# Kernel optimization log

Measured on AMD Instinct MI355X. Metric: run time of the kernel, lower is better.

The kernel has to match this reference:

```python
import jax, jax.numpy as jnp
import numpy as np

BATCH, TOK, DIM, OUT = 4, 2048, 4096, 4096
E, R, TOP_K = 8, 16, 2
SCALING = 16.0 / R  # lora_alpha / r


def setup_inputs() -> dict:
    key = jax.random.key(0)
    ks = jax.random.split(key, 6)
    return {
        "x": jax.random.normal(ks[0], (BATCH, TOK, DIM), dtype=jnp.float32),
        "W_base": jax.random.normal(ks[1], (OUT, DIM), dtype=jnp.float32) / np.sqrt(DIM),
        "b_base": jax.random.normal(ks[2], (OUT,), dtype=jnp.float32) * 0.01,
        "W_gate": jax.random.normal(ks[3], (E, DIM), dtype=jnp.float32) * 0.01,
        "A": jax.random.normal(ks[4], (E, R, DIM), dtype=jnp.float32) / np.sqrt(DIM),
        "B": jax.random.normal(ks[5], (OUT, OUT // OUT * R * 0 + R), dtype=jnp.float32)[None].repeat(E, 0) * 0.0 + jax.random.normal(ks[5], (E, OUT, R), dtype=jnp.float32) * 0.02,
    }


def reference(x, W_base, b_base, W_gate, A, B):
    # Base frozen linear: [B,N,D] @ [D,O] -> [B,N,O]
    result = jnp.einsum("bnd,od->bno", x, W_base) + b_base
    # Gating
    logits = jnp.einsum("bnd,ed->bne", x, W_gate)
    probs = jax.nn.softmax(logits.astype(jnp.float32), axis=-1)  # fp32 softmax
    top_p, top_i = jax.lax.top_k(probs, TOP_K)  # [B,N,K]
    top_p = top_p / jnp.sum(top_p, axis=-1, keepdims=True)  # top_k > 1 branch
    top_p = top_p.astype(x.dtype)
    # Scatter top-k probs back to dense [B,N,E] routing weights
    route_w = jnp.sum(jax.nn.one_hot(top_i, E, dtype=x.dtype) * top_p[..., None], axis=-2)
    # Per-expert LoRA: down-project all tokens for all experts (r is small),
    # weight by routing, then up-project and sum over experts.
    h = jnp.einsum("bnd,erd->bner", x, A)          # [B,N,E,r]
    hw = h * route_w[..., None]                      # mask/combine weighting
    delta = jnp.einsum("bner,eor->bno", hw, B)      # [B,N,O]
    return result + delta * SCALING
```

## Files before the change

kernel.cpp:

```cpp
#include <hip/hip_runtime.h>
#include <hip/hip_bf16.h>
#include <cstdint>

#define TOKENS 8192
#define DIM_   4096
#define OUTD   4096
#define NE     8
#define NR     16
#define LORA_COLS (NE*NR)
#define KCAT  (DIM_ + LORA_COLS)
#define NTILES (KCAT/64)
#define HSPLIT 8
#define HKC    (DIM_/HSPLIT)

typedef __attribute__((ext_vector_type(8))) short short8;
typedef __attribute__((ext_vector_type(4))) float f32x4;

__device__ __forceinline__ unsigned short f2bf(float f) {
  union { float f; unsigned u; } v; v.f = f;
  unsigned r = v.u + 0x7FFFu + ((v.u >> 16) & 1u);
  return (unsigned short)(r >> 16);
}
__device__ __forceinline__ float bf2f(unsigned short u) {
  union { unsigned u; float f; } v; v.u = ((unsigned)u) << 16; return v.f;
}

__device__ __forceinline__ void load_lds16(const void* g, void* l) {
  auto gp = reinterpret_cast<const __attribute__((address_space(1))) unsigned int*>(
      reinterpret_cast<uintptr_t>(g));
  auto lp = reinterpret_cast<__attribute__((address_space(3))) unsigned int*>(
      reinterpret_cast<uintptr_t>(l));
  __builtin_amdgcn_global_load_lds(gp, lp, 16, 0, 0);
}

#define BAR() asm volatile("s_barrier" ::: "memory")
#define LGKM(N) do { asm volatile("s_waitcnt lgkmcnt(" #N ")" ::: "memory"); \
                     __builtin_amdgcn_sched_barrier(0); } while (0)
#define VMW(N) asm volatile("s_waitcnt vmcnt(" #N ")" ::: "memory")
#define SB0() __builtin_amdgcn_sched_barrier(0)

__global__ __launch_bounds__(256) void fused_prep_kernel(
    const float* __restrict__ x, const float* __restrict__ Wg,
    const float* __restrict__ W, const float* __restrict__ Bm,
    const float* __restrict__ Am, unsigned short* __restrict__ Wcat,
    unsigned short* __restrict__ Acat, unsigned short* __restrict__ Xcat,
    int* __restrict__ ridx, float* __restrict__ rw, float scaling) {
  __shared__ float red[32 * 257];
  __shared__ float lg[32];
  int tid = threadIdx.x;
  int bb = blockIdx.x;
  if (bb < OUTD) {
    const float4* src = (const float4*)(W + (size_t)bb * DIM_);
    unsigned short* dst = Wcat + (size_t)bb * KCAT;
#pragma unroll
    for (int j = 0; j < DIM_ / 1024; ++j) {
      float4 v = src[j * 256 + tid];
      ushort4 o; o.x = f2bf(v.x); o.y = f2bf(v.y); o.z = f2bf(v.z); o.w = f2bf(v.w);
      *(ushort4*)(dst + (size_t)(j * 256 + tid) * 4) = o;
    }
    if (tid < LORA_COLS) {
      int e = tid >> 4, r = tid & 15;
      dst[DIM_ + tid] = f2bf(scaling * Bm[((size_t)e * OUTD + bb) * NR + r]);
    }
    return;
  }
  if (bb < OUTD + LORA_COLS) {
    int i = bb - OUTD;
    const float4* src = (const float4*)(Am + (size_t)i * DIM_);
    unsigned short* dst = Acat + (size_t)i * DIM_;
#pragma unroll
    for (int j = 0; j < DIM_ / 1024; ++j) {
      float4 v = src[j * 256 + tid];
      ushort4 o; o.x = f2bf(v.x); o.y = f2bf(v.y); o.z = f2bf(v.z); o.w = f2bf(v.w);
      *(ushort4*)(dst + (size_t)(j * 256 + tid) * 4) = o;
    }
    return;
  }
  int t0 = (bb - OUTD - LORA_COLS) * 4;
  float acc[4][8];
#pragma unroll
  for (int ti = 0; ti < 4; ++ti)
#pragma unroll
    for (int e = 0; e < 8; ++e) acc[ti][e] = 0.f;
  const float4* x4 = (const float4*)x;
  const float4* wg4 = (const float4*)Wg;
#pragma unroll
  for (int j = 0; j < 4; ++j) {
    int dpos = j * 256 + tid;
    float4 wg[8];
#pragma unroll
    for (int e = 0; e < 8; ++e) wg[e] = wg4[e * 1024 + dpos];
#pragma unroll
    for (int ti = 0; ti < 4; ++ti) {
      float4 v = x4[(size_t)(t0 + ti) * 1024 + dpos];
      ushort4 o; o.x = f2bf(v.x); o.y = f2bf(v.y); o.z = f2bf(v.z); o.w = f2bf(v.w);
      *(ushort4*)&Xcat[(size_t)(t0 + ti) * KCAT + (size_t)dpos * 4] = o;
#pragma unroll
      for (int e = 0; e < 8; ++e)
        acc[ti][e] += v.x * wg[e].x + v.y * wg[e].y + v.z * wg[e].z + v.w * wg[e].w;
    }
  }
#pragma unroll
  for (int p = 0; p < 32; ++p) red[p * 257 + tid] = acc[p >> 3][p & 7];
  __syncthreads();
  {
    int p = tid >> 3, part = tid & 7;
    float s = 0.f;
#pragma unroll
    for (int i = 0; i < 32; ++i) s += red[p * 257 + part * 32 + i];
    s += __shfl_xor(s, 1);
    s += __shfl_xor(s, 2);
    s += __shfl_xor(s, 4);
    if (part == 0) lg[p] = s;
  }
  __syncthreads();
  if (tid < 4) {
    float l[8];
#pragma unroll
    for (int e = 0; e < 8; ++e) l[e] = lg[tid * 8 + e];
    int i0 = 0; float m0 = l[0];
#pragma unroll
    for (int e = 1; e < 8; ++e) if (l[e] > m0) { m0 = l[e]; i0 = e; }
    int i1 = -1; float m1 = -3.4e38f;
#pragma unroll
    for (int e = 0; e < 8; ++e) if (e != i0 && l[e] > m1) { m1 = l[e]; i1 = e; }
    float w0 = 1.0f / (1.0f + expf(m1 - m0));
    int t = t0 + tid;
    ridx[t * 2] = i0; ridx[t * 2 + 1] = i1;
    rw[t * 2] = w0;  rw[t * 2 + 1] = 1.0f - w0;
  }
}

template <int MODE>
__global__ __launch_bounds__(256) void gemm_kernel(
    const unsigned short* __restrict__ Aop, const unsigned short* __restrict__ Bop,
    float* __restrict__ Cout, unsigned short* __restrict__ CoutBf,
    const float* __restrict__ bias, const int* __restrict__ ridx,
    const float* __restrict__ rw,
    int M, int N, int K, int lda, int ldb, int ldc) {
  __shared__ __align__(16) unsigned short lsA[128 * 32];
  __shared__ __align__(16) unsigned short lsB[128 * 32];
  int tid = threadIdx.x;
  int lane = tid & 63, wave = tid >> 6;
  int wm = wave >> 1, wn = wave & 1;
  int row0 = blockIdx.x * 128, col0 = blockIdx.y * 128;

  f32x4 acc[4][4];
#pragma unroll
  for (int a = 0; a < 4; ++a)
#pragma unroll
    for (int b = 0; b < 4; ++b) acc[a][b] = (f32x4){0.f, 0.f, 0.f, 0.f};

  int lrow = lane >> 2;
  int lcol = (lane & 3) << 3;
  int fr = lane & 15, fk = (lane >> 4) << 3;

  const unsigned short* gA0 = Aop + (size_t)(row0 + wave * 32 + lrow) * lda + lcol;
  const unsigned short* gA1 = Aop + (size_t)(row0 + wave * 32 + 16 + lrow) * lda + lcol;
  const unsigned short* gB0 = Bop + (size_t)(col0 + wave * 32 + lrow) * ldb + lcol;
  const unsigned short* gB1 = Bop + (size_t)(col0 + wave * 32 + 16 + lrow) * ldb + lcol;

  for (int k0 = 0; k0 < K; k0 += 32) {
    load_lds16(gA0 + k0, lsA + wave * 1024);
    load_lds16(gA1 + k0, lsA + wave * 1024 + 512);
    load_lds16(gB0 + k0, lsB + wave * 1024);
    load_lds16(gB1 + k0, lsB + wave * 1024 + 512);
    __syncthreads();
    short8 af[4], bfr[4];
#pragma unroll
    for (int mi = 0; mi < 4; ++mi)
      af[mi] = *(const short8*)&lsA[(wm * 64 + mi * 16 + fr) * 32 + fk];
#pragma unroll
    for (int ni = 0; ni < 4; ++ni)
      bfr[ni] = *(const short8*)&lsB[(wn * 64 + ni * 16 + fr) * 32 + fk];
#pragma unroll
    for (int mi = 0; mi < 4; ++mi)
#pragma unroll
      for (int ni = 0; ni < 4; ++ni)
        acc[mi][ni] = __builtin_amdgcn_mfma_f32_16x16x32_bf16(af[mi], bfr[ni], acc[mi][ni], 0, 0, 0);
    __syncthreads();
  }

  int fg = lane >> 4;
  if (MODE == 0) {
#pragma unroll
    for (int ni = 0; ni < 4; ++ni) {
      int col = col0 + wn * 64 + ni * 16 + fr;
      float bv = bias[col];
#pragma unroll
      for (int mi = 0; mi < 4; ++mi)
#pragma unroll
        for (int j = 0; j < 4; ++j) {
          int row = row0 + wm * 64 + mi * 16 + fg * 4 + j;
          Cout[(size_t)row * ldc + col] = acc[mi][ni][j] + bv;
        }
    }
  } else {
#pragma unroll
    for (int mi = 0; mi < 4; ++mi)
#pragma unroll
      for (int j = 0; j < 4; ++j) {
        int row = row0 + wm * 64 + mi * 16 + fg * 4 + j;
        int i0 = ridx[row * 2], i1 = ridx[row * 2 + 1];
        float w0 = rw[row * 2], w1 = rw[row * 2 + 1];
#pragma unroll
        for (int ni = 0; ni < 4; ++ni) {
          int col = wn * 64 + ni * 16 + fr;
          int e = col >> 4;
          float w = (e == i0) ? w0 : ((e == i1) ? w1 : 0.f);
          CoutBf[(size_t)row * ldc + col] = f2bf(w * acc[mi][ni][j]);
        }
      }
  }
}

__global__ __launch_bounds__(256) void gemm_h_sk_kernel(
    const unsigned short* __restrict__ Aop,
    const unsigned short* __restrict__ Bop,
    unsigned short* __restrict__ Hpart) {
  __shared__ __align__(16) unsigned short lsA[128 * 32];
  __shared__ __align__(16) unsigned short lsB[128 * 32];
  int tid = threadIdx.x;
  int lane = tid & 63, wave = tid >> 6;
  int wm = wave >> 1, wn = wave & 1;
  int row0 = blockIdx.x * 128;
  int s = blockIdx.y;
  int kbeg = s * HKC;

  f32x4 acc[4][4];
#pragma unroll
  for (int a = 0; a < 4; ++a)
#pragma unroll
    for (int b = 0; b < 4; ++b) acc[a][b] = (f32x4){0.f, 0.f, 0.f, 0.f};

  int lrow = lane >> 2;
  int lcol = (lane & 3) << 3;
  int fr = lane & 15, fk = (lane >> 4) << 3;

  const unsigned short* gA0 = Aop + (size_t)(row0 + wave * 32 + lrow) * KCAT + lcol;
  const unsigned short* gA1 = Aop + (size_t)(row0 + wave * 32 + 16 + lrow) * KCAT + lcol;
  const unsigned short* gB0 = Bop + (size_t)(wave * 32 + lrow) * DIM_ + lcol;
  const unsigned short* gB1 = Bop + (size_t)(wave * 32 + 16 + lrow) * DIM_ + lcol;

  for (int k0 = kbeg; k0 < kbeg + HKC; k0 += 32) {
    load_lds16(gA0 + k0, lsA + wave * 1024);
    load_lds16(gA1 + k0, lsA + wave * 1024 + 512);
    load_lds16(gB0 + k0, lsB + wave * 1024);
    load_lds16(gB1 + k0, lsB + wave * 1024 + 512);
    __syncthreads();
    short8 af[4], bfr[4];
#pragma unroll
    for (int mi = 0; mi < 4; ++mi)
      af[mi] = *(const short8*)&lsA[(wm * 64 + mi * 16 + fr) * 32 + fk];
#pragma unroll
    for (int ni = 0; ni < 4; ++ni)
      bfr[ni] = *(const short8*)&lsB[(wn * 64 + ni * 16 + fr) * 32 + fk];
#pragma unroll
    for (int mi = 0; mi < 4; ++mi)
#pragma unroll
      for (int ni = 0; ni < 4; ++ni)
        acc[mi][ni] = __builtin_amdgcn_mfma_f32_16x16x32_bf16(af[mi], bfr[ni], acc[mi][ni], 0, 0, 0);
    __syncthreads();
  }

  int fg = lane >> 4;
  unsigned short* outp = Hpart + (size_t)s * TOKENS * 128;
#pragma unroll
  for (int ni = 0; ni < 4; ++ni) {
    int col = wn * 64 + ni * 16 + fr;
#pragma unroll
    for (int mi = 0; mi < 4; ++mi)
#pragma unroll
      for (int j = 0; j < 4; ++j) {
        int row = row0 + wm * 64 + mi * 16 + fg * 4 + j;
        outp[(size_t)row * 128 + col] = f2bf(acc[mi][ni][j]);
      }
  }
}

__global__ __launch_bounds__(256) void h_combine_kernel(
    const unsigned short* __restrict__ Hpart, const int* __restrict__ ridx,
    const float* __restrict__ rw, unsigned short* __restrict__ Xcat) {
  int gid = blockIdx.x * 256 + threadIdx.x;
  int t = gid >> 7, c = gid & 127;
  float s = 0.f;
#pragma unroll
  for (int i = 0; i < HSPLIT; ++i) s += bf2f(Hpart[(size_t)i * TOKENS * 128 + gid]);
  int e = c >> 4;
  int i0 = ridx[t * 2], i1 = ridx[t * 2 + 1];
  float w = (e == i0) ? rw[t * 2] : ((e == i1) ? rw[t * 2 + 1] : 0.f);
  Xcat[(size_t)t * KCAT + DIM_ + c] = f2bf(w * s);
}

#define RD_A4(dst, base, ks, mi0) do { \
  dst[0] = *(const short8*)((base) + (((mi0)+0)*2+(ks))*1024); \
  dst[1] = *(const short8*)((base) + (((mi0)+1)*2+(ks))*1024); \
  dst[2] = *(const short8*)((base) + (((mi0)+2)*2+(ks))*1024); \
  dst[3] = *(const short8*)((base) + (((mi0)+3)*2+(ks))*1024); } while (0)
#define RD_B4(dst, base, ks) do { \
  dst[0] = *(const short8*)((base) + 0*2048 + (ks)*1024); \
  dst[1] = *(const short8*)((base) + 1*2048 + (ks)*1024); \
  dst[2] = *(const short8*)((base) + 2*2048 + (ks)*1024); \
  dst[3] = *(const short8*)((base) + 3*2048 + (ks)*1024); } while (0)
#define MFMA_H(a4, b4, m0, mo) do { \
  __builtin_amdgcn_s_setprio(1); \
  _Pragma("unroll") \
  for (int mi = 0; mi < 2; ++mi) { \
    _Pragma("unroll") \
    for (int ni = 0; ni < 4; ++ni) { \
      acc[(m0)+(mo)+mi][ni] = __builtin_amdgcn_mfma_f32_16x16x32_bf16( \
          b4[ni], a4[(mo)+mi], acc[(m0)+(mo)+mi][ni], 0, 0, 0); } } \
  __builtin_amdgcn_s_setprio(0); } while (0)
#define STAGE(srcp, kofs, dst) do { \
  load_lds16((srcp) + (kofs), (dst)); \
  load_lds16((srcp) + (kofs) + 32, (dst) + 1024); } while (0)

__global__ __launch_bounds__(512, 2) void gemm256_kernel(
    const unsigned short* __restrict__ Aop,
    const unsigned short* __restrict__ Bop,
    float* __restrict__ Cout, const float* __restrict__ bias) {
  extern __shared__ char lds[];
  const int tid = threadIdx.x;
  const int lane = tid & 63, wave = tid >> 6;
  const int wm = wave >> 2, wn = wave & 3;
  const int fr = lane & 15, kg = lane >> 4;

  const int bid = blockIdx.x;
  const int swz = (bid & 7) * 64 + (bid >> 3);
  const int mt = swz >> 4, nt = swz & 15;
  const int row0 = mt * 256, nt0 = nt * 256;
  const int col0 = nt0;

  const int srow = lane >> 2;
  const int scol = ((lane & 3) * 8) ^ (((lane >> 5) & 1) * 16);
  const unsigned short* sA0 = Aop + (size_t)(row0 +       wave * 16 + srow) * KCAT + scol;
  const unsigned short* sA1 = Aop + (size_t)(row0 + 128 + wave * 16 + srow) * KCAT + scol;
  const unsigned short* sB0 = Bop + (size_t)(col0 +       wave * 16 + srow) * KCAT + scol;
  const unsigned short* sB1 = Bop + (size_t)(col0 + 128 + wave * 16 + srow) * KCAT + scol;

  char* dA0b0 = lds +      0 + wave * 2048;
  char* dA1b0 = lds +  16384 + wave * 2048;
  char* dB0b0 = lds +  32768 + wave * 2048;
  char* dB1b0 = lds +  49152 + wave * 2048;
  char* dA0b1 = dA0b0 + 65536;
  char* dA1b1 = dA1b0 + 65536;
  char* dB0b1 = dB0b0 + 65536;
  char* dB1b1 = dB1b0 + 65536;

  const int swzo = (kg * 16) ^ ((fr >> 3) << 5);
  const char* rdA0 = lds + wm * 16384 + fr * 64 + swzo;
  const char* rdA1 = rdA0 + 65536;
  const char* rdB0 = lds + 32768 + (wn >> 1) * 16384 + (wn & 1) * 8192 + fr * 64 + swzo;
  const char* rdB1 = rdB0 + 65536;

  f32x4 acc[8][4];
#pragma unroll
  for (int a = 0; a < 8; ++a)
#pragma unroll
    for (int b = 0; b < 4; ++b) acc[a][b] = (f32x4){0.f, 0.f, 0.f, 0.f};

  short8 aL[4], aH[4], a1L[4], a1H[4], b0f[4], b1f[4];

  STAGE(sA0, 0, dA0b0); STAGE(sA1, 0, dA1b0);
  STAGE(sB0, 0, dB0b0); STAGE(sB1, 0, dB1b0);
  STAGE(sB0, 64, dB0b1); STAGE(sB1, 64, dB1b1); STAGE(sA0, 64, dA0b1);
  VMW(6);
  BAR();
  RD_A4(aL, rdA0, 0, 0); RD_B4(b0f, rdB0, 0);

  for (int i = 0; i < NTILES / 2 - 1; ++i) {
    const int k1 = (2 * i + 1) * 64, k2 = k1 + 64, k3 = k1 + 128;
    STAGE(sA1, k1, dA1b1);
    BAR(); LGKM(0);
    MFMA_H(aL, b0f, 0, 0);
    SB0(); RD_A4(aH, rdA0, 0, 4); RD_B4(b1f, rdB0, 1); SB0();
    MFMA_H(aL, b0f, 0, 2);
    BAR();
    STAGE(sB0, k2, dB0b0);
    BAR(); LGKM(4);
    MFMA_H(aH, b0f, 4, 0);
    SB0(); RD_A4(a1L, rdA0, 1, 0); SB0();
    MFMA_H(aH, b0f, 4, 2);
    BAR();
    STAGE(sB1, k2, dB1b0);
    BAR(); LGKM(0);
    MFMA_H(a1L, b1f, 0, 0);
    SB0(); RD_A4(a1H, rdA0, 1, 4); SB0();
    MFMA_H(a1L, b1f, 0, 2);
    BAR();
    STAGE(sA0, k2, dA0b0);
    VMW(6);
    BAR(); LGKM(0);
    MFMA_H(a1H, b1f, 4, 0);
    SB0(); RD_A4(aL, rdA1, 0, 0); RD_B4(b0f, rdB1, 0); SB0();
    MFMA_H(a1H, b1f, 4, 2);
    BAR();
    STAGE(sA1, k2, dA1b0);
    BAR(); LGKM(0);
    MFMA_H(aL, b0f, 0, 0);
    SB0(); RD_A4(aH, rdA1, 0, 4); RD_B4(b1f, rdB1, 1); SB0();
    MFMA_H(aL, b0f, 0, 2);
    BAR();
    STAGE(sB0, k3, dB0b1);
    BAR(); LGKM(4);
    MFMA_H(aH, b0f, 4, 0);
    SB0(); RD_A4(a1L, rdA1, 1, 0); SB0();
    MFMA_H(aH, b0f, 4, 2);
    BAR();
    STAGE(sB1, k3, dB1b1);
    BAR(); LGKM(0);
    MFMA_H(a1L, b1f, 0, 0);
    SB0(); RD_A4(a1H, rdA1, 1, 4); SB0();
    MFMA_H(a1L, b1f, 0, 2);
    BAR();
    STAGE(sA0, k3, dA0b1);
    VMW(6);
    BAR(); LGKM(0);
    MFMA_H(a1H, b1f, 4, 0);
    SB0(); RD_A4(aL, rdA0, 0, 0); RD_B4(b0f, rdB0, 0); SB0();
    MFMA_H(a1H, b1f, 4, 2);
    BAR();
  }

  {
    const int k65 = 65 * 64;
    STAGE(sA1, k65, dA1b1);
    BAR(); LGKM(0);
    MFMA_H(aL, b0f, 0, 0);
    SB0(); RD_A4(aH, rdA0, 0, 4); RD_B4(b1f, rdB0, 1); SB0();
    MFMA_H(aL, b0f, 0, 2);
    BAR();
    BAR(); LGKM(4);
    MFMA_H(aH, b0f, 4, 0);
    SB0(); RD_A4(a1L, rdA0, 1, 0); SB0();
    MFMA_H(aH, b0f, 4, 2);
    BAR();
    BAR(); LGKM(0);
    MFMA_H(a1L, b1f, 0, 0);
    SB0(); RD_A4(a1H, rdA0, 1, 4); SB0();
    MFMA_H(a1L, b1f, 0, 2);
    BAR();
    VMW(0);
    BAR(); LGKM(0);
    MFMA_H(a1H, b1f, 4, 0);
    SB0(); RD_A4(aL, rdA1, 0, 0); RD_B4(b0f, rdB1, 0); SB0();
    MFMA_H(a1H, b1f, 4, 2);
    BAR();
    LGKM(0);
    MFMA_H(aL, b0f, 0, 0); MFMA_H(aL, b0f, 0, 2);
    RD_A4(aH, rdA1, 0, 4); RD_B4(b1f, rdB1, 1);
    LGKM(0);
    MFMA_H(aH, b0f, 4, 0); MFMA_H(aH, b0f, 4, 2);
    RD_A4(a1L, rdA1, 1, 0); RD_A4(a1H, rdA1, 1, 4);
    LGKM(4);
    MFMA_H(a1L, b1f, 0, 0); MFMA_H(a1L, b1f, 0, 2);
    LGKM(0);
    MFMA_H(a1H, b1f, 4, 0); MFMA_H(a1H, b1f, 4, 2);
  }

#pragma unroll
  for (int ni = 0; ni < 4; ++ni) {
    int colb = col0 + wn * 64 + ni * 16 + kg * 4;
    float4 bv = *(const float4*)&bias[colb];
#pragma unroll
    for (int mi = 0; mi < 8; ++mi) {
      int row = row0 + wm * 128 + mi * 16 + fr;
      float4 v;
      v.x = acc[mi][ni][0] + bv.x;
      v.y = acc[mi][ni][1] + bv.y;
      v.z = acc[mi][ni][2] + bv.z;
      v.w = acc[mi][ni][3] + bv.w;
      *(float4*)&Cout[(size_t)row * OUTD + colb] = v;
    }
  }
}

extern "C" void kernel_launch(void* const* d_in, const int* in_sizes, int n_in,
                              void* d_out, int out_size, void* d_ws, size_t ws_size,
                              hipStream_t stream) {
  const float* x  = (const float*)d_in[0];
  const float* Wb = (const float*)d_in[1];
  const float* bb = (const float*)d_in[2];
  const float* Wg = (const float*)d_in[3];
  const float* Am = (const float*)d_in[4];
  const float* Bm = (const float*)d_in[5];
  float* out = (float*)d_out;

  unsigned short* Wcat = (unsigned short*)d_ws;
  unsigned short* Xcat = Wcat + (size_t)OUTD * KCAT;
  unsigned short* Acat = Xcat + (size_t)TOKENS * KCAT;
  int*   ridx = (int*)(Acat + (size_t)LORA_COLS * DIM_);
  float* rw   = (float*)(ridx + (size_t)TOKENS * 2);
  unsigned short* Hpart = (unsigned short*)(rw + (size_t)TOKENS * 2);

  const size_t ws_needed = (size_t)((char*)(Hpart + (size_t)HSPLIT * TOKENS * 128)
                                    - (char*)d_ws);
  const bool use_splitk = (ws_size >= ws_needed);

  const float scaling = 16.0f / (float)NR;

  hipFuncSetAttribute((const void*)gemm256_kernel,
                      hipFuncAttributeMaxDynamicSharedMemorySize, 131072);

  fused_prep_kernel<<<dim3(OUTD + LORA_COLS + TOKENS / 4), dim3(256), 0, stream>>>(
      x, Wg, Wb, Bm, Am, Wcat, Acat, Xcat, ridx, rw, scaling);
  if (use_splitk) {
    gemm_h_sk_kernel<<<dim3(TOKENS / 128, HSPLIT), dim3(256), 0, stream>>>(
        Xcat, Acat, Hpart);
    h_combine_kernel<<<dim3(TOKENS * 128 / 256), dim3(256), 0, stream>>>(
        Hpart, ridx, rw, Xcat);
  } else {
    gemm_kernel<1><<<dim3(TOKENS / 128, 1), dim3(256), 0, stream>>>(
        Xcat, Acat, (float*)nullptr, Xcat + DIM_, (const float*)nullptr,
        ridx, rw, TOKENS, LORA_COLS, DIM_, KCAT, DIM_, KCAT);
  }
  gemm256_kernel<<<dim3(512), dim3(512), 131072, stream>>>(Xcat, Wcat, out, bb);
}
```

Measured before the change: 310.4 us.

## Reschedule GEMM main loop for deeper LDS read prefetch and fewer barriers

Restructures the software pipeline of the 256x256 bf16 MFMA GEMM. A-operand halves are now staged in pairs, and LDS fragment reads are issued one phase further ahead, using partial lgkmcnt waits (4 or 8) instead of full drains. Some redundant barriers are dropped and the prologue and epilogue are reworked to match. The aim is more overlap of LDS and global traffic with MFMA work, at the risk of subtle race or ordering bugs if the wait counts or buffer reuse are wrong.

```diff
diff --git a/kernel.cpp b/kernel.cpp
--- a/kernel.cpp
+++ b/kernel.cpp
@@ -328,8 +328,7 @@
   const int bid = blockIdx.x;
   const int swz = (bid & 7) * 64 + (bid >> 3);
   const int mt = swz >> 4, nt = swz & 15;
-  const int row0 = mt * 256, nt0 = nt * 256;
-  const int col0 = nt0;
+  const int row0 = mt * 256, col0 = nt * 256;
 
   const int srow = lane >> 2;
   const int scol = ((lane & 3) * 8) ^ (((lane >> 5) & 1) * 16);
@@ -363,99 +362,104 @@
 
   STAGE(sA0, 0, dA0b0); STAGE(sA1, 0, dA1b0);
   STAGE(sB0, 0, dB0b0); STAGE(sB1, 0, dB1b0);
-  STAGE(sB0, 64, dB0b1); STAGE(sB1, 64, dB1b1); STAGE(sA0, 64, dA0b1);
-  VMW(6);
+  STAGE(sB0, 64, dB0b1); STAGE(sB1, 64, dB1b1);
+  VMW(4);
   BAR();
   RD_A4(aL, rdA0, 0, 0); RD_B4(b0f, rdB0, 0);
-
-  for (int i = 0; i < NTILES / 2 - 1; ++i) {
+  RD_A4(aH, rdA0, 0, 4);
+
+  for (int i = 0; i < 32; ++i) {
     const int k1 = (2 * i + 1) * 64, k2 = k1 + 64, k3 = k1 + 128;
-    STAGE(sA1, k1, dA1b1);
-    BAR(); LGKM(0);
+    LGKM(4);
     MFMA_H(aL, b0f, 0, 0);
-    SB0(); RD_A4(aH, rdA0, 0, 4); RD_B4(b1f, rdB0, 1); SB0();
+    SB0(); RD_A4(a1L, rdA0, 1, 0); RD_B4(b1f, rdB0, 1); SB0();
     MFMA_H(aL, b0f, 0, 2);
-    BAR();
+    STAGE(sA0, k1, dA0b1); STAGE(sA1, k1, dA1b1);
+    BAR();
+    LGKM(8);
+    MFMA_H(aH, b0f, 4, 0);
+    SB0(); RD_A4(a1H, rdA0, 1, 4); SB0();
+    MFMA_H(aH, b0f, 4, 2);
     STAGE(sB0, k2, dB0b0);
-    BAR(); LGKM(4);
+    VMW(2);
+    BAR();
+    LGKM(4);
+    MFMA_H(a1L, b1f, 0, 0);
+    SB0(); RD_A4(aL, rdA1, 0, 0); RD_B4(b0f, rdB1, 0); SB0();
+    MFMA_H(a1L, b1f, 0, 2);
+    BAR();
+    LGKM(8);
+    MFMA_H(a1H, b1f, 4, 0);
+    SB0(); RD_A4(aH, rdA1, 0, 4); SB0();
+    MFMA_H(a1H, b1f, 4, 2);
+    STAGE(sB1, k2, dB1b0);
+    BAR();
+    LGKM(4);
+    MFMA_H(aL, b0f, 0, 0);
+    SB0(); RD_A4(a1L, rdA1, 1, 0); RD_B4(b1f, rdB1, 1); SB0();
+    MFMA_H(aL, b0f, 0, 2);
+    STAGE(sA0, k2, dA0b0); STAGE(sA1, k2, dA1b0);
+    BAR();
+    LGKM(8);
     MFMA_H(aH, b0f, 4, 0);
-    SB0(); RD_A4(a1L, rdA0, 1, 0); SB0();
+    SB0(); RD_A4(a1H, rdA1, 1, 4); SB0();
     MFMA_H(aH, b0f, 4, 2);
-    BAR();
-    STAGE(sB1, k2, dB1b0);
-    BAR(); LGKM(0);
+    STAGE(sB0, k3, dB0b1);
+    VMW(2);
+    BAR();
+    LGKM(4);
     MFMA_H(a1L, b1f, 0, 0);
-    SB0(); RD_A4(a1H, rdA0, 1, 4); SB0();
+    SB0(); RD_A4(aL, rdA0, 0, 0); RD_B4(b0f, rdB0, 0); SB0();
     MFMA_H(a1L, b1f, 0, 2);
     BAR();
-    STAGE(sA0, k2, dA0b0);
-    VMW(6);
-    BAR(); LGKM(0);
+    LGKM(8);
     MFMA_H(a1H, b1f, 4, 0);
-    SB0(); RD_A4(aL, rdA1, 0, 0); RD_B4(b0f, rdB1, 0); SB0();
+    SB0(); RD_A4(aH, rdA0, 0, 4); SB0();
     MFMA_H(a1H, b1f, 4, 2);
-    BAR();
-    STAGE(sA1, k2, dA1b0);
-    BAR(); LGKM(0);
-    MFMA_H(aL, b0f, 0, 0);
-    SB0(); RD_A4(aH, rdA1, 0, 4); RD_B4(b1f, rdB1, 1); SB0();
-    MFMA_H(aL, b0f, 0, 2);
-    BAR();
-    STAGE(sB0, k3, dB0b1);
-    BAR(); LGKM(4);
-    MFMA_H(aH, b0f, 4, 0);
-    SB0(); RD_A4(a1L, rdA1, 1, 0); SB0();
-    MFMA_H(aH, b0f, 4, 2);
-    BAR();
     STAGE(sB1, k3, dB1b1);
-    BAR(); LGKM(0);
-    MFMA_H(a1L, b1f, 0, 0);
-    SB0(); RD_A4(a1H, rdA1, 1, 4); SB0();
-    MFMA_H(a1L, b1f, 0, 2);
-    BAR();
-    STAGE(sA0, k3, dA0b1);
-    VMW(6);
-    BAR(); LGKM(0);
-    MFMA_H(a1H, b1f, 4, 0);
-    SB0(); RD_A4(aL, rdA0, 0, 0); RD_B4(b0f, rdB0, 0); SB0();
-    MFMA_H(a1H, b1f, 4, 2);
     BAR();
   }
 
   {
     const int k65 = 65 * 64;
-    STAGE(sA1, k65, dA1b1);
-    BAR(); LGKM(0);
+    LGKM(4);
     MFMA_H(aL, b0f, 0, 0);
-    SB0(); RD_A4(aH, rdA0, 0, 4); RD_B4(b1f, rdB0, 1); SB0();
+    SB0(); RD_A4(a1L, rdA0, 1, 0); RD_B4(b1f, rdB0, 1); SB0();
     MFMA_H(aL, b0f, 0, 2);
-    BAR();
-    BAR(); LGKM(4);
+    STAGE(sA0, k65, dA0b1); STAGE(sA1, k65, dA1b1);
+    BAR();
+    LGKM(8);
     MFMA_H(aH, b0f, 4, 0);
-    SB0(); RD_A4(a1L, rdA0, 1, 0); SB0();
+    SB0(); RD_A4(a1H, rdA0, 1, 4); SB0();
     MFMA_H(aH, b0f, 4, 2);
-    BAR();
-    BAR(); LGKM(0);
+    VMW(0);
+    BAR();
+    LGKM(4);
     MFMA_H(a1L, b1f, 0, 0);
-    SB0(); RD_A4(a1H, rdA0, 1, 4); SB0();
+    SB0(); RD_A4(aL, rdA1, 0, 0); RD_B4(b0f, rdB1, 0); SB0();
     MFMA_H(a1L, b1f, 0, 2);
     BAR();
-    VMW(0);
-    BAR(); LGKM(0);
+    LGKM(8);
     MFMA_H(a1H, b1f, 4, 0);
-    SB0(); RD_A4(aL, rdA1, 0, 0); RD_B4(b0f, rdB1, 0); SB0();
+    SB0(); RD_A4(aH, rdA1, 0, 4); SB0();
     MFMA_H(a1H, b1f, 4, 2);
     BAR();
+    LGKM(4);
+    MFMA_H(aL, b0f, 0, 0);
+    SB0(); RD_A4(a1L, rdA1, 1, 0); RD_B4(b1f, rdB1, 1); SB0();
+    MFMA_H(aL, b0f, 0, 2);
+    BAR();
+    LGKM(8);
+    MFMA_H(aH, b0f, 4, 0);
+    SB0(); RD_A4(a1H, rdA1, 1, 4); SB0();
+    MFMA_H(aH, b0f, 4, 2);
+    BAR();
+    LGKM(4);
+    MFMA_H(a1L, b1f, 0, 0);
+    MFMA_H(a1L, b1f, 0, 2);
     LGKM(0);
-    MFMA_H(aL, b0f, 0, 0); MFMA_H(aL, b0f, 0, 2);
-    RD_A4(aH, rdA1, 0, 4); RD_B4(b1f, rdB1, 1);
-    LGKM(0);
-    MFMA_H(aH, b0f, 4, 0); MFMA_H(aH, b0f, 4, 2);
-    RD_A4(a1L, rdA1, 1, 0); RD_A4(a1H, rdA1, 1, 4);
-    LGKM(4);
-    MFMA_H(a1L, b1f, 0, 0); MFMA_H(a1L, b1f, 0, 2);
-    LGKM(0);
-    MFMA_H(a1H, b1f, 4, 0); MFMA_H(a1H, b1f, 4, 2);
+    MFMA_H(a1H, b1f, 4, 0);
+    MFMA_H(a1H, b1f, 4, 2);
   }
 
 #pragma unroll
```

Measured after the change: 333.5 us. 7.5% more time.
